# Kernel tuning notes

Hardware: AMD Instinct MI355X
Metric: run time of the kernel (lower is better)

## Reference

```python
import jax, jax.numpy as jnp
import numpy as np


def _unfold2d(x, side):
    # x: (B, C, H, W) -> (B, C, out, out, side, side), stride-1 sliding windows
    H = x.shape[2]
    out = H - side + 1
    idx = jnp.arange(out)[:, None] + jnp.arange(side)[None, :]  # (out, side)
    x = x[:, :, idx, :]        # (B, C, out, side, W)
    x = x[:, :, :, :, idx]     # (B, C, out, side, out, side)
    return jnp.transpose(x, (0, 1, 2, 4, 3, 5))  # (B, C, out, out, side, side)


def setup_inputs() -> dict:
    key = jax.random.key(0)
    k1, k2, k3 = jax.random.split(key, 3)
    img, side, num = 128, 5, 25
    out = img - side + 1  # 124
    x = jax.random.normal(k1, (1, 3, img, img), dtype=jnp.float32)
    w = jax.random.normal(k2, (3, out, out, num, side, side), dtype=jnp.float32)
    q = jax.random.normal(k3, (3, out, out, num, side, side), dtype=jnp.float32)
    return {"x": x, "w": w, "q": q}


def reference(x, w, q):
    side = w.shape[-1]
    # patches: (1, 3, out, out, 1, side, side) -- broadcast replaces torch repeat
    p = _unfold2d(x, side)[:, :, :, :, None, :, :]
    y = (jnp.pi + 2.0 * jnp.arctan(10.0 * (p * w - q))) / (2.0 * jnp.pi)
    y = jnp.log(jnp.prod(y + 0.6, axis=6))  # product over last window dim, then log
    y = jnp.sum(y, axis=5)                   # sum over remaining window dim
    return y  # (1, 3, out, out, num)
```

## Files before the change

kernel.cpp:

```cpp
#include <hip/hip_runtime.h>


#define IMG   128
#define OUT   124
#define NUM   25
#define NOUT  (3 * OUT * OUT * NUM)
#define OPB   256

__device__ __forceinline__ float fast_atan(float z) {
    float az  = __builtin_fabsf(z);
    float r   = __builtin_amdgcn_rcpf(az);
    bool  big = az > 1.0f;
    float t   = big ? r : az;
    float s   = t * t;
    float p   =                     -0.01172120f;
    p = __builtin_fmaf(p, s,         0.05265332f);
    p = __builtin_fmaf(p, s,        -0.11643287f);
    p = __builtin_fmaf(p, s,         0.19354346f);
    p = __builtin_fmaf(p, s,        -0.33262347f);
    p = __builtin_fmaf(p, s,         0.99997726f);
    float a = t * p;
    a = big ? (1.57079632679489662f - a) : a;
    return __builtin_copysignf(a, z);
}

__device__ __forceinline__ float4 load4u(const float* p) {
    float4 v;
    __builtin_memcpy(&v, p, sizeof(float4));
    return v;
}

__global__ __launch_bounds__(OPB) void dendrite_kernel(
    const float* __restrict__ x,
    const float* __restrict__ w,
    const float* __restrict__ q,
    float* __restrict__ out)
{
    const int o = blockIdx.x * OPB + threadIdx.x;
    if (o >= NOUT) return;

    int rem = o / NUM;
    const int j = rem % OUT;  rem /= OUT;
    const int i = rem % OUT;
    const int c = rem / OUT;

    const float* wp = w + (long long)o * NUM;
    const float* qp = q + (long long)o * NUM;
    const float* xp = x + ((long long)c * IMG + i) * IMG + j;

    float wv[NUM], qv[NUM], xv[NUM];
    #pragma unroll
    for (int g = 0; g < 6; ++g) {
        float4 a = load4u(wp + 4 * g);
        wv[4*g+0] = a.x; wv[4*g+1] = a.y; wv[4*g+2] = a.z; wv[4*g+3] = a.w;
    }
    wv[24] = wp[24];
    #pragma unroll
    for (int g = 0; g < 6; ++g) {
        float4 a = load4u(qp + 4 * g);
        qv[4*g+0] = a.x; qv[4*g+1] = a.y; qv[4*g+2] = a.z; qv[4*g+3] = a.w;
    }
    qv[24] = qp[24];
    #pragma unroll
    for (int u = 0; u < 5; ++u) {
        float4 a = load4u(xp + u * IMG);
        xv[5*u+0] = a.x; xv[5*u+1] = a.y; xv[5*u+2] = a.z; xv[5*u+3] = a.w;
        xv[5*u+4] = xp[u * IMG + 4];
    }

    float prod0 = 1.0f, prod1 = 1.0f;
    #pragma unroll
    for (int k = 0; k < NUM; ++k) {
        const float z = 10.0f * __builtin_fmaf(xv[k], wv[k], -qv[k]);
        const float a = fast_atan(z);
        const float term = __builtin_fmaf(a, 0.31830988618379067f, 1.1f);
        if (k & 1) prod1 *= term; else prod0 *= term;
    }
    out[o] = __logf(prod0 * prod1);
}

extern "C" void kernel_launch(void* const* d_in, const int* in_sizes, int n_in,
                              void* d_out, int out_size, void* d_ws, size_t ws_size,
                              hipStream_t stream) {
    const float* x = (const float*)d_in[0];
    const float* w = (const float*)d_in[1];
    const float* q = (const float*)d_in[2];
    float* out = (float*)d_out;

    const int grid = (NOUT + OPB - 1) / OPB;
    dendrite_kernel<<<grid, OPB, 0, stream>>>(x, w, q, out);
}
```

Measured before the change: 246.5 us.

## Stage w and q through LDS with coalesced global_load_lds per wave

Each wave now loads its contiguous 64x25 slice of w and q with coalesced 16-byte direct global-to-LDS loads instead of per-thread strided vector loads. Threads then read their 25 weights from LDS. This targets the poorly coalesced, misaligned per-thread float4 loads, at the cost of LDS usage (about 50KB per block), which may limit occupancy, plus possible LDS bank conflicts from the stride-25 reads.

```diff
diff --git a/kernel.cpp b/kernel.cpp
--- a/kernel.cpp
+++ b/kernel.cpp
@@ -5,7 +5,10 @@
 #define OUT   124
 #define NUM   25
 #define NOUT  (3 * OUT * OUT * NUM)
-#define OPB   256
+#define WTOT  ((long long)NOUT * NUM)
+#define WPB   4
+#define OPB   (WPB * 64)
+#define FPW   (64 * NUM)
 
 __device__ __forceinline__ float fast_atan(float z) {
     float az  = __builtin_fabsf(z);
@@ -24,10 +27,15 @@
     return __builtin_copysignf(a, z);
 }
 
-__device__ __forceinline__ float4 load4u(const float* p) {
-    float4 v;
-    __builtin_memcpy(&v, p, sizeof(float4));
-    return v;
+__device__ __forceinline__ void gl_lds16(const float* g, float* l) {
+    __builtin_amdgcn_global_load_lds(
+        (const __attribute__((address_space(1))) unsigned int*)g,
+        (__attribute__((address_space(3))) unsigned int*)l, 16, 0, 0);
+}
+__device__ __forceinline__ void gl_lds4(const float* g, float* l) {
+    __builtin_amdgcn_global_load_lds(
+        (const __attribute__((address_space(1))) unsigned int*)g,
+        (__attribute__((address_space(3))) unsigned int*)l, 4, 0, 0);
 }
 
 __global__ __launch_bounds__(OPB) void dendrite_kernel(
@@ -36,42 +44,66 @@
     const float* __restrict__ q,
     float* __restrict__ out)
 {
-    const int o = blockIdx.x * OPB + threadIdx.x;
-    if (o >= NOUT) return;
+    __shared__ float lw[WPB][FPW];
+    __shared__ float lq[WPB][FPW];
 
-    int rem = o / NUM;
+    const int lane = threadIdx.x & 63;
+    const int wv   = threadIdx.x >> 6;
+    const long long wave_id = (long long)blockIdx.x * WPB + wv;
+    const long long wo      = wave_id * 64;
+    const long long fbase   = wo * NUM;
+
+    #pragma unroll
+    for (int it = 0; it < 6; ++it) {
+        long long gi = fbase + it * 256 + lane * 4;
+        if (gi > WTOT - 4) gi = WTOT - 4;
+        gl_lds16(w + gi, &lw[wv][it * 256 + lane * 4]);
+    }
+    {
+        long long gi = fbase + 1536 + lane;
+        if (gi > WTOT - 1) gi = WTOT - 1;
+        gl_lds4(w + gi, &lw[wv][1536 + lane]);
+    }
+    #pragma unroll
+    for (int it = 0; it < 6; ++it) {
+        long long gi = fbase + it * 256 + lane * 4;
+        if (gi > WTOT - 4) gi = WTOT - 4;
+        gl_lds16(q + gi, &lq[wv][it * 256 + lane * 4]);
+    }
+    {
+        long long gi = fbase + 1536 + lane;
+        if (gi > WTOT - 1) gi = WTOT - 1;
+        gl_lds4(q + gi, &lq[wv][1536 + lane]);
+    }
+
+    const long long o = wo + lane;
+    const bool live = (o < NOUT);
+    int rem = live ? (int)(o / NUM) : 0;
     const int j = rem % OUT;  rem /= OUT;
     const int i = rem % OUT;
     const int c = rem / OUT;
-
-    const float* wp = w + (long long)o * NUM;
-    const float* qp = q + (long long)o * NUM;
     const float* xp = x + ((long long)c * IMG + i) * IMG + j;
 
-    float wv[NUM], qv[NUM], xv[NUM];
-    #pragma unroll
-    for (int g = 0; g < 6; ++g) {
-        float4 a = load4u(wp + 4 * g);
-        wv[4*g+0] = a.x; wv[4*g+1] = a.y; wv[4*g+2] = a.z; wv[4*g+3] = a.w;
-    }
-    wv[24] = wp[24];
-    #pragma unroll
-    for (int g = 0; g < 6; ++g) {
-        float4 a = load4u(qp + 4 * g);
-        qv[4*g+0] = a.x; qv[4*g+1] = a.y; qv[4*g+2] = a.z; qv[4*g+3] = a.w;
-    }
-    qv[24] = qp[24];
+    float xv[NUM];
     #pragma unroll
     for (int u = 0; u < 5; ++u) {
-        float4 a = load4u(xp + u * IMG);
+        float4 a;
+        __builtin_memcpy(&a, xp + u * IMG, sizeof(float4));
         xv[5*u+0] = a.x; xv[5*u+1] = a.y; xv[5*u+2] = a.z; xv[5*u+3] = a.w;
         xv[5*u+4] = xp[u * IMG + 4];
     }
 
+    asm volatile("s_waitcnt vmcnt(0)" ::: "memory");
+
+    if (!live) return;
+
+    const float* wp = &lw[wv][lane * NUM];
+    const float* qp = &lq[wv][lane * NUM];
+
     float prod0 = 1.0f, prod1 = 1.0f;
     #pragma unroll
     for (int k = 0; k < NUM; ++k) {
-        const float z = 10.0f * __builtin_fmaf(xv[k], wv[k], -qv[k]);
+        const float z = 10.0f * __builtin_fmaf(xv[k], wp[k], -qp[k]);
         const float a = fast_atan(z);
         const float term = __builtin_fmaf(a, 0.31830988618379067f, 1.1f);
         if (k & 1) prod1 *= term; else prod0 *= term;
```

Result: no change. 247.2 us (+0.3%).

## Coalesce w/q loads per wavefront and transpose through LDS with prefetch

Applied to the files above, without the earlier changes.

Each wavefront now streams contiguous 1600-float chunks of w and q using lane-strided float4 loads instead of per-thread 25-float strided reads. It computes a log term per element, stages the terms in LDS and reduces 25 of them per output. Each wave handles three chunks, loading the next chunk before computing the current one so memory latency is overlapped. In exchange it adds per-element index div/mod arithmetic and 25 logs per output instead of one, and it changes the numerics from the log of a product to a sum of logs.

```diff
diff --git a/kernel.cpp b/kernel.cpp
--- a/kernel.cpp
+++ b/kernel.cpp
@@ -1,11 +1,17 @@
 #include <hip/hip_runtime.h>
 
 
-#define IMG   128
-#define OUT   124
-#define NUM   25
-#define NOUT  (3 * OUT * OUT * NUM)
-#define OPB   256
+#define IMG    128
+#define OUTD   124
+#define NUM    25
+#define NOUT   (3 * OUTD * OUTD * NUM)
+#define WTOT   28830000u
+#define CHUNK  1600u
+#define NCHUNK 18019u
+#define WPB    4
+#define OPB    (WPB * 64)
+#define CPW    3
+#define NBLK   1504
 
 __device__ __forceinline__ float fast_atan(float z) {
     float az  = __builtin_fabsf(z);
@@ -24,59 +30,99 @@
     return __builtin_copysignf(a, z);
 }
 
-__device__ __forceinline__ float4 load4u(const float* p) {
-    float4 v;
-    __builtin_memcpy(&v, p, sizeof(float4));
-    return v;
+__device__ __forceinline__ float log_term(const float* __restrict__ x,
+                                          unsigned e, float wv, float qv) {
+    const unsigned ee = e < (WTOT - 1u) ? e : (WTOT - 1u);
+    const unsigned v  = ee % 5u;
+    const unsigned u  = (ee / 5u) % 5u;
+    const unsigned m  = ee / 625u;
+    const unsigned j  = m % 124u;
+    const unsigned t  = m / 124u;
+    const unsigned i_ = t % 124u;
+    const unsigned ci = t / 124u;
+    const float xv = x[ci * (IMG * IMG) + (i_ + u) * IMG + (j + v)];
+    const float z  = 10.0f * __builtin_fmaf(xv, wv, -qv);
+    const float a  = fast_atan(z);
+    const float term = __builtin_fmaf(a, 0.31830988618379067f, 1.1f);
+    const float lt = __logf(term);
+    return e < WTOT ? lt : 0.0f;
 }
 
-__global__ __launch_bounds__(OPB) void dendrite_kernel(
+__device__ __forceinline__ void load_chunk(unsigned c,
+    const float* __restrict__ w, const float* __restrict__ q, int lane,
+    float4 W[6], float4 Q[6], float& Wt, float& Qt) {
+    const unsigned base = c * CHUNK;
+    #pragma unroll
+    for (int i = 0; i < 6; ++i) {
+        unsigned gi = base + 256u * i + 4u * lane;
+        if (gi > WTOT - 4u) gi = WTOT - 4u;
+        W[i] = *(const float4*)(w + gi);
+        Q[i] = *(const float4*)(q + gi);
+    }
+    unsigned gt = base + 1536u + lane;
+    if (gt > WTOT - 1u) gt = WTOT - 1u;
+    Wt = w[gt];
+    Qt = q[gt];
+}
+
+__global__ __launch_bounds__(OPB, 3) void dendrite_kernel(
     const float* __restrict__ x,
     const float* __restrict__ w,
     const float* __restrict__ q,
     float* __restrict__ out)
 {
-    const int o = blockIdx.x * OPB + threadIdx.x;
-    if (o >= NOUT) return;
+    __shared__ float lds[WPB][CHUNK];
 
-    int rem = o / NUM;
-    const int j = rem % OUT;  rem /= OUT;
-    const int i = rem % OUT;
-    const int c = rem / OUT;
+    const int lane = threadIdx.x & 63;
+    const int wib  = threadIdx.x >> 6;
+    const unsigned wgid = blockIdx.x * WPB + wib;
+    const unsigned c0   = wgid * CPW;
+    if (c0 >= NCHUNK) return;
 
-    const float* wp = w + (long long)o * NUM;
-    const float* qp = q + (long long)o * NUM;
-    const float* xp = x + ((long long)c * IMG + i) * IMG + j;
+    float4 W[6], Q[6]; float Wt, Qt;
+    load_chunk(c0, w, q, lane, W, Q, Wt, Qt);
 
-    float wv[NUM], qv[NUM], xv[NUM];
     #pragma unroll
-    for (int g = 0; g < 6; ++g) {
-        float4 a = load4u(wp + 4 * g);
-        wv[4*g+0] = a.x; wv[4*g+1] = a.y; wv[4*g+2] = a.z; wv[4*g+3] = a.w;
+    for (int s = 0; s < CPW; ++s) {
+        const unsigned c = c0 + s;
+        if (c >= NCHUNK) break;
+
+        float4 Wn[6], Qn[6]; float Wtn = 0.0f, Qtn = 0.0f;
+        const bool pf = (s + 1 < CPW) && (c + 1 < NCHUNK);
+        if (pf) load_chunk(c + 1, w, q, lane, Wn, Qn, Wtn, Qtn);
+
+        const unsigned base = c * CHUNK;
+        #pragma unroll
+        for (int i = 0; i < 6; ++i) {
+            const unsigned el0 = 256u * i + 4u * lane;
+            const float* wf = (const float*)&W[i];
+            const float* qf = (const float*)&Q[i];
+            float lt[4];
+            #pragma unroll
+            for (int jj = 0; jj < 4; ++jj)
+                lt[jj] = log_term(x, base + el0 + jj, wf[jj], qf[jj]);
+            *(float4*)&lds[wib][el0] = make_float4(lt[0], lt[1], lt[2], lt[3]);
+        }
+        lds[wib][1536u + lane] = log_term(x, base + 1536u + lane, Wt, Qt);
+
+        __asm volatile("s_waitcnt lgkmcnt(0)" ::: "memory");
+
+        float sum = 0.0f;
+        #pragma unroll
+        for (int k = 0; k < NUM; ++k)
+            sum += lds[wib][lane * NUM + k];
+
+        const unsigned o = c * 64u + lane;
+        if (o < (unsigned)NOUT) out[o] = sum;
+
+        __asm volatile("" ::: "memory");
+
+        if (pf) {
+            #pragma unroll
+            for (int i = 0; i < 6; ++i) { W[i] = Wn[i]; Q[i] = Qn[i]; }
+            Wt = Wtn; Qt = Qtn;
+        }
     }
-    wv[24] = wp[24];
-    #pragma unroll
-    for (int g = 0; g < 6; ++g) {
-        float4 a = load4u(qp + 4 * g);
-        qv[4*g+0] = a.x; qv[4*g+1] = a.y; qv[4*g+2] = a.z; qv[4*g+3] = a.w;
-    }
-    qv[24] = qp[24];
-    #pragma unroll
-    for (int u = 0; u < 5; ++u) {
-        float4 a = load4u(xp + u * IMG);
-        xv[5*u+0] = a.x; xv[5*u+1] = a.y; xv[5*u+2] = a.z; xv[5*u+3] = a.w;
-        xv[5*u+4] = xp[u * IMG + 4];
-    }
-
-    float prod0 = 1.0f, prod1 = 1.0f;
-    #pragma unroll
-    for (int k = 0; k < NUM; ++k) {
-        const float z = 10.0f * __builtin_fmaf(xv[k], wv[k], -qv[k]);
-        const float a = fast_atan(z);
-        const float term = __builtin_fmaf(a, 0.31830988618379067f, 1.1f);
-        if (k & 1) prod1 *= term; else prod0 *= term;
-    }
-    out[o] = __logf(prod0 * prod1);
 }
 
 extern "C" void kernel_launch(void* const* d_in, const int* in_sizes, int n_in,
@@ -87,6 +133,5 @@
     const float* q = (const float*)d_in[2];
     float* out = (float*)d_out;
 
-    const int grid = (NOUT + OPB - 1) / OPB;
-    dendrite_kernel<<<grid, OPB, 0, stream>>>(x, w, q, out);
+    dendrite_kernel<<<NBLK, OPB, 0, stream>>>(x, w, q, out);
 }
```

Measured after the change: 260.5 us. 5.7% more time.

## Stage coalesced w/q chunk loads through LDS with persistent register-prefetched waves

Applied to the files above, without the earlier changes.

Each wave now owns a contiguous 1600-float chunk of w and q, covering 64 outputs. The chunk is read with lane-contiguous float4 loads, written to LDS, and then each lane reads its own 25 elements back. This replaces the old pattern where every thread issued unaligned, strided 100-byte loads that coalesced poorly. The grid becomes a fixed persistent launch where each wave walks several chunks and prefetches the next chunk into registers while computing the current one. The cost is LDS traffic, higher register pressure and occupancy limits, and clamped indexing that makes some tail work redundant.

```diff
diff --git a/kernel.cpp b/kernel.cpp
--- a/kernel.cpp
+++ b/kernel.cpp
@@ -1,11 +1,17 @@
 #include <hip/hip_runtime.h>
 
 
-#define IMG   128
-#define OUT   124
-#define NUM   25
-#define NOUT  (3 * OUT * OUT * NUM)
-#define OPB   256
+#define IMG    128
+#define OUTD   124
+#define NUM    25
+#define NOUT   1153200
+#define WTOT   28830000u
+#define NCHUNK 18019u
+#define WPB    4
+#define OPB    256
+#define NBLK   768
+#define NWAVE  3072u
+#define ITERS  6
 
 __device__ __forceinline__ float fast_atan(float z) {
     float az  = __builtin_fabsf(z);
@@ -24,59 +30,89 @@
     return __builtin_copysignf(a, z);
 }
 
-__device__ __forceinline__ float4 load4u(const float* p) {
-    float4 v;
-    __builtin_memcpy(&v, p, sizeof(float4));
-    return v;
+struct ChunkRegs { float4 W[6]; float4 Q[6]; float Wt, Qt; };
+
+__device__ __forceinline__ void load_chunk(unsigned ch,
+    const float* __restrict__ w, const float* __restrict__ q, int lane,
+    ChunkRegs& r) {
+    const unsigned base = ch * 1600u;
+    #pragma unroll
+    for (int it = 0; it < 6; ++it) {
+        unsigned gi = base + 256u * it + 4u * lane;
+        gi = gi > WTOT - 4u ? WTOT - 4u : gi;
+        r.W[it] = *(const float4*)(w + gi);
+        r.Q[it] = *(const float4*)(q + gi);
+    }
+    unsigned gt = base + 1536u + lane;
+    gt = gt > WTOT - 1u ? WTOT - 1u : gt;
+    r.Wt = w[gt];
+    r.Qt = q[gt];
 }
 
-__global__ __launch_bounds__(OPB) void dendrite_kernel(
+__global__ __launch_bounds__(OPB, 3) void dendrite_kernel(
     const float* __restrict__ x,
     const float* __restrict__ w,
     const float* __restrict__ q,
     float* __restrict__ out)
 {
-    const int o = blockIdx.x * OPB + threadIdx.x;
-    if (o >= NOUT) return;
+    __shared__ float lw[WPB][1600];
+    __shared__ float lq[WPB][1600];
 
-    int rem = o / NUM;
-    const int j = rem % OUT;  rem /= OUT;
-    const int i = rem % OUT;
-    const int c = rem / OUT;
+    const int lane = threadIdx.x & 63;
+    const int wv   = threadIdx.x >> 6;
+    const unsigned g = blockIdx.x * WPB + wv;
 
-    const float* wp = w + (long long)o * NUM;
-    const float* qp = q + (long long)o * NUM;
-    const float* xp = x + ((long long)c * IMG + i) * IMG + j;
+    ChunkRegs cur;
+    load_chunk(g, w, q, lane, cur);
 
-    float wv[NUM], qv[NUM], xv[NUM];
     #pragma unroll
-    for (int g = 0; g < 6; ++g) {
-        float4 a = load4u(wp + 4 * g);
-        wv[4*g+0] = a.x; wv[4*g+1] = a.y; wv[4*g+2] = a.z; wv[4*g+3] = a.w;
+    for (int s = 0; s < ITERS; ++s) {
+        unsigned ch = g + (unsigned)s * NWAVE;
+        ch = ch < NCHUNK ? ch : NCHUNK - 1u;
+
+        #pragma unroll
+        for (int it = 0; it < 6; ++it) {
+            *(float4*)&lw[wv][256 * it + 4 * lane] = cur.W[it];
+            *(float4*)&lq[wv][256 * it + 4 * lane] = cur.Q[it];
+        }
+        lw[wv][1536 + lane] = cur.Wt;
+        lq[wv][1536 + lane] = cur.Qt;
+
+        const int o  = (int)(ch * 64u) + lane;
+        const int oc = o < NOUT ? o : NOUT - 1;
+        const int m  = oc / NUM;
+        const int j  = m % OUTD;
+        const int t2 = m / OUTD;
+        const int i  = t2 % OUTD;
+        const int cc = t2 / OUTD;
+        const float* xp = x + (cc * IMG + i) * IMG + j;
+        float xv[NUM];
+        #pragma unroll
+        for (int u = 0; u < 5; ++u) {
+            float4 a;
+            __builtin_memcpy(&a, xp + u * IMG, sizeof(float4));
+            xv[5*u+0] = a.x; xv[5*u+1] = a.y; xv[5*u+2] = a.z; xv[5*u+3] = a.w;
+            xv[5*u+4] = xp[u * IMG + 4];
+        }
+
+        if (s + 1 < ITERS) {
+            unsigned chn = g + (unsigned)(s + 1) * NWAVE;
+            chn = chn < NCHUNK ? chn : NCHUNK - 1u;
+            load_chunk(chn, w, q, lane, cur);
+        }
+
+        const float* wp = &lw[wv][lane * NUM];
+        const float* qp = &lq[wv][lane * NUM];
+        float prod0 = 1.0f, prod1 = 1.0f;
+        #pragma unroll
+        for (int k = 0; k < NUM; ++k) {
+            const float z = 10.0f * __builtin_fmaf(xv[k], wp[k], -qp[k]);
+            const float a = fast_atan(z);
+            const float term = __builtin_fmaf(a, 0.31830988618379067f, 1.1f);
+            if (k & 1) prod1 *= term; else prod0 *= term;
+        }
+        if (o < NOUT) out[o] = __logf(prod0 * prod1);
     }
-    wv[24] = wp[24];
-    #pragma unroll
-    for (int g = 0; g < 6; ++g) {
-        float4 a = load4u(qp + 4 * g);
-        qv[4*g+0] = a.x; qv[4*g+1] = a.y; qv[4*g+2] = a.z; qv[4*g+3] = a.w;
-    }
-    qv[24] = qp[24];
-    #pragma unroll
-    for (int u = 0; u < 5; ++u) {
-        float4 a = load4u(xp + u * IMG);
-        xv[5*u+0] = a.x; xv[5*u+1] = a.y; xv[5*u+2] = a.z; xv[5*u+3] = a.w;
-        xv[5*u+4] = xp[u * IMG + 4];
-    }
-
-    float prod0 = 1.0f, prod1 = 1.0f;
-    #pragma unroll
-    for (int k = 0; k < NUM; ++k) {
-        const float z = 10.0f * __builtin_fmaf(xv[k], wv[k], -qv[k]);
-        const float a = fast_atan(z);
-        const float term = __builtin_fmaf(a, 0.31830988618379067f, 1.1f);
-        if (k & 1) prod1 *= term; else prod0 *= term;
-    }
-    out[o] = __logf(prod0 * prod1);
 }
 
 extern "C" void kernel_launch(void* const* d_in, const int* in_sizes, int n_in,
@@ -87,6 +123,5 @@
     const float* q = (const float*)d_in[2];
     float* out = (float*)d_out;
 
-    const int grid = (NOUT + OPB - 1) / OPB;
-    dendrite_kernel<<<grid, OPB, 0, stream>>>(x, w, q, out);
+    dendrite_kernel<<<NBLK, OPB, 0, stream>>>(x, w, q, out);
 }
```

New measurement: 251.5 us. 1.02x slower.
